# Performance work log

Hardware: AMD Instinct MI355X
Metric: run time of the kernel (lower is better)

The kernel has to match this reference:

```python
import jax, jax.numpy as jnp
import numpy as np
import math

B, S, E, H = 2, 8192, 1024, 16
D = E // H  # 64
CHUNK = 128


def _build_slopes(n):
    # ALiBi-style slopes (n is a power of 2 here)
    start = 2.0 ** (-(2.0 ** -(math.log2(n) - 3)))
    return np.array([start * (start ** i) for i in range(n)], dtype=np.float32)


def setup_inputs() -> dict:
    key = jax.random.key(0)
    ks = jax.random.split(key, 6)
    x = jax.random.normal(ks[0], (B, S, E), dtype=jnp.float32)
    # rotary table: (S, D//2, 2) = (cos, sin)
    inv_freq = 1.0 / (10000.0 ** (np.arange(0, D, 2, dtype=np.float32) / D))
    ang = np.arange(S, dtype=np.float32)[:, None] * inv_freq[None, :]  # (S, D/2)
    freqs_cis = jnp.asarray(np.stack([np.cos(ang), np.sin(ang)], axis=-1))
    wq = jax.random.normal(ks[1], (E, E), dtype=jnp.float32) * 0.02
    wk = jax.random.normal(ks[2], (E, E), dtype=jnp.float32) * 0.02
    wv = jax.random.normal(ks[3], (E, E), dtype=jnp.float32) * 0.02
    wo = jax.random.normal(ks[4], (E, E), dtype=jnp.float32) * 0.02
    rms_w = jnp.ones((E,), dtype=jnp.float32)
    return {"x": x, "freqs_cis": freqs_cis, "wq": wq, "wk": wk, "wv": wv, "wo": wo, "rms_w": rms_w}


def apply_rotary(x, fc):
    # x: (b, s, h, d); fc: (s, d/2, 2)
    xr = x.reshape(*x.shape[:-1], -1, 2)          # (b,s,h,d/2,2)
    fc = fc[None, :, None, :, :]                   # (1,s,1,d/2,2)
    out = jnp.stack([
        xr[..., 0] * fc[..., 0] - xr[..., 1] * fc[..., 1],
        xr[..., 1] * fc[..., 0] + xr[..., 0] * fc[..., 1],
    ], axis=-1)
    return out.reshape(x.shape)


def lightning_attn(q, k, v, slopes, C=CHUNK):
    # q,k,v: (B,H,S,D); per-head decay lambda = exp(-slope)
    Bs, Hs, Ss, Ds = q.shape
    NC = Ss // C
    j = jnp.arange(C, dtype=jnp.float32)
    diff = j[:, None] - j[None, :]
    s3 = slopes[:, None, None]                     # (H,1,1)
    Dmask = jnp.where(diff >= 0, jnp.exp(-s3 * diff), 0.0)   # (H,C,C) intra decay
    q_dec = jnp.exp(-slopes[:, None] * (j + 1.0))             # (H,C) cross-chunk q decay
    k_dec = jnp.exp(-slopes[:, None] * (C - 1.0 - j))         # (H,C) state-update k decay
    c_dec = jnp.exp(-slopes * C)[None, :, None, None]         # (1,H,1,1) full-chunk decay
    qc = q.reshape(Bs, Hs, NC, C, Ds).transpose(2, 0, 1, 3, 4)
    kc = k.reshape(Bs, Hs, NC, C, Ds).transpose(2, 0, 1, 3, 4)
    vc = v.reshape(Bs, Hs, NC, C, Ds).transpose(2, 0, 1, 3, 4)

    def step(St, inp):
        qb, kb, vb = inp                                       # (B,H,C,D)
        scores = jnp.einsum('bhid,bhjd->bhij', qb, kb) * Dmask[None]
        o = jnp.einsum('bhij,bhjd->bhid', scores, vb)
        o = o + q_dec[None, :, :, None] * jnp.einsum('bhid,bhde->bhie', qb, St)
        St = c_dec * St + jnp.einsum('bhcd,bhce->bhde', kb * k_dec[None, :, :, None], vb)
        return St, o

    S0 = jnp.zeros((Bs, Hs, Ds, Ds), dtype=jnp.float32)
    _, oc = jax.lax.scan(step, S0, (qc, kc, vc))               # oc: (NC,B,H,C,D)
    return oc.transpose(1, 2, 0, 3, 4).reshape(Bs, Hs, Ss, Ds)


def rms_norm(x, w, eps=1e-5):
    xf = x.astype(jnp.float32)
    n = xf * jax.lax.rsqrt(jnp.mean(xf * xf, axis=-1, keepdims=True) + eps)
    return n.astype(x.dtype) * w


def reference(x, freqs_cis, wq, wk, wv, wo, rms_w):
    b, s, _ = x.shape
    slopes = jnp.asarray(_build_slopes(H))
    q = (x @ wq.T).reshape(b, s, H, D)
    k = (x @ wk.T).reshape(b, s, H, D)
    v = (x @ wv.T).reshape(b, s, H, D)
    q = apply_rotary(q, freqs_cis)
    k = apply_rotary(k, freqs_cis)
    q = q.transpose(0, 2, 1, 3)   # (B,H,S,D)
    k = k.transpose(0, 2, 1, 3)
    v = v.transpose(0, 2, 1, 3)
    o = lightning_attn(q, k, v, slopes)             # (B,H,S,D)
    o = o.transpose(0, 2, 1, 3).reshape(b, s, E)    # b n (h d)
    o = rms_norm(o, rms_w)
    return o @ wo.T
```

## Files before the change

kernel.cpp:

```cpp
#include <hip/hip_runtime.h>


using h16   = _Float16;
using h16x8 = __attribute__((ext_vector_type(8))) _Float16;
using h16x4 = __attribute__((ext_vector_type(4))) _Float16;
using f32x4 = __attribute__((ext_vector_type(4))) float;

#define MFMA16(a,b,c) __builtin_amdgcn_mfma_f32_16x16x32_f16(a,b,c,0,0,0)

__device__ __forceinline__ h16x8 rope8(h16x8 v, const float* __restrict__ fp) {
  float4 f0 = *(const float4*)fp;
  float4 f1 = *(const float4*)(fp + 4);
  h16x8 o; float x0, x1;
  x0=(float)v[0]; x1=(float)v[1]; o[0]=(h16)(x0*f0.x - x1*f0.y); o[1]=(h16)(x1*f0.x + x0*f0.y);
  x0=(float)v[2]; x1=(float)v[3]; o[2]=(h16)(x0*f0.z - x1*f0.w); o[3]=(h16)(x1*f0.z + x0*f0.w);
  x0=(float)v[4]; x1=(float)v[5]; o[4]=(h16)(x0*f1.x - x1*f1.y); o[5]=(h16)(x1*f1.x + x0*f1.y);
  x0=(float)v[6]; x1=(float)v[7]; o[6]=(h16)(x0*f1.z - x1*f1.w); o[7]=(h16)(x1*f1.z + x0*f1.w);
  return o;
}

__global__ __launch_bounds__(256) void k_cvt(const float* __restrict__ s,
                                             h16* __restrict__ d, int n) {
  int i = (blockIdx.x * 256 + threadIdx.x) * 8;
  if (i >= n) return;
  float4 a = *(const float4*)(s + i);
  float4 b = *(const float4*)(s + i + 4);
  h16x8 o;
  o[0]=(h16)a.x; o[1]=(h16)a.y; o[2]=(h16)a.z; o[3]=(h16)a.w;
  o[4]=(h16)b.x; o[5]=(h16)b.y; o[6]=(h16)b.z; o[7]=(h16)b.w;
  *(h16x8*)(d + i) = o;
}

__global__ __launch_bounds__(256) void k_qkv(
    const h16* __restrict__ xh, const h16* __restrict__ w3,
    h16* __restrict__ qn, h16* __restrict__ kn, h16* __restrict__ vn)
{
  __shared__ __align__(16) h16 lA[128*64];
  __shared__ __align__(16) h16 lB[128*64];
  const int tid = threadIdx.x;
  const int m0 = blockIdx.x * 128;
  const int nt = blockIdx.y;
  const int n0 = nt * 128;
  const int w = tid >> 6, l = tid & 63;
  const int wr = w >> 1, wc = w & 1;
  const int sr = tid >> 3, sc = tid & 7;
  const int ssl = sc ^ (sr & 7);
  const h16* At = xh + (size_t)m0 * 1024;
  const h16* Bt = w3 + (size_t)n0 * 1024;

  f32x4 acc[4][4] = {};
  h16x8 ra[4], rb[4];
  #pragma unroll
  for (int i = 0; i < 4; i++) {
    ra[i] = *(const h16x8*)(At + (size_t)(i*32+sr)*1024 + sc*8);
    rb[i] = *(const h16x8*)(Bt + (size_t)(i*32+sr)*1024 + sc*8);
  }
  #pragma unroll
  for (int i = 0; i < 4; i++) {
    *(h16x8*)(lA + (i*32+sr)*64 + ssl*8) = ra[i];
    *(h16x8*)(lB + (i*32+sr)*64 + ssl*8) = rb[i];
  }
  __syncthreads();

  for (int kt = 0; kt < 16; ++kt) {
    if (kt < 15) {
      #pragma unroll
      for (int i = 0; i < 4; i++) {
        ra[i] = *(const h16x8*)(At + (size_t)(i*32+sr)*1024 + (kt+1)*64 + sc*8);
        rb[i] = *(const h16x8*)(Bt + (size_t)(i*32+sr)*1024 + (kt+1)*64 + sc*8);
      }
    }
    #pragma unroll
    for (int ks = 0; ks < 2; ++ks) {
      h16x8 af[4], bf[4];
      #pragma unroll
      for (int mf = 0; mf < 4; mf++) {
        int row = wr*64 + mf*16 + (l & 15);
        int slot = (ks*4 + (l >> 4)) ^ (row & 7);
        af[mf] = *(const h16x8*)(lA + row*64 + slot*8);
      }
      #pragma unroll
      for (int nf = 0; nf < 4; nf++) {
        int row = wc*64 + nf*16 + (l & 15);
        int slot = (ks*4 + (l >> 4)) ^ (row & 7);
        bf[nf] = *(const h16x8*)(lB + row*64 + slot*8);
      }
      #pragma unroll
      for (int mf = 0; mf < 4; mf++)
        #pragma unroll
        for (int nf = 0; nf < 4; nf++)
          acc[mf][nf] = MFMA16(af[mf], bf[nf], acc[mf][nf]);
    }
    __syncthreads();
    if (kt < 15) {
      #pragma unroll
      for (int i = 0; i < 4; i++) {
        *(h16x8*)(lA + (i*32+sr)*64 + ssl*8) = ra[i];
        *(h16x8*)(lB + (i*32+sr)*64 + ssl*8) = rb[i];
      }
    }
    __syncthreads();
  }

  const int proj = nt >> 3;
  h16* dst = proj == 0 ? qn : (proj == 1 ? kn : vn);
  const int cb = (nt & 7) * 128;
  #pragma unroll
  for (int mf = 0; mf < 4; mf++)
    #pragma unroll
    for (int nf = 0; nf < 4; nf++)
      #pragma unroll
      for (int r = 0; r < 4; r++) {
        int row = wr*64 + mf*16 + ((l >> 4) << 2) + r;
        int col = cb + wc*64 + nf*16 + (l & 15);
        dst[(size_t)(m0 + row)*1024 + col] = (h16)acc[mf][nf][r];
      }
}

__global__ __launch_bounds__(256) void k_out(
    const h16* __restrict__ an, const h16* __restrict__ woh,
    float* __restrict__ out)
{
  __shared__ __align__(16) h16 lA[128*64];
  __shared__ __align__(16) h16 lB[128*64];
  const int tid = threadIdx.x;
  const int m0 = blockIdx.x * 128;
  const int n0 = blockIdx.y * 128;
  const int w = tid >> 6, l = tid & 63;
  const int wr = w >> 1, wc = w & 1;
  const int sr = tid >> 3, sc = tid & 7;
  const int ssl = sc ^ (sr & 7);
  const h16* At = an + (size_t)m0 * 1024;
  const h16* Bt = woh + (size_t)n0 * 1024;

  f32x4 acc[4][4] = {};
  h16x8 ra[4], rb[4];
  #pragma unroll
  for (int i = 0; i < 4; i++) {
    ra[i] = *(const h16x8*)(At + (size_t)(i*32+sr)*1024 + sc*8);
    rb[i] = *(const h16x8*)(Bt + (size_t)(i*32+sr)*1024 + sc*8);
  }
  #pragma unroll
  for (int i = 0; i < 4; i++) {
    *(h16x8*)(lA + (i*32+sr)*64 + ssl*8) = ra[i];
    *(h16x8*)(lB + (i*32+sr)*64 + ssl*8) = rb[i];
  }
  __syncthreads();

  for (int kt = 0; kt < 16; ++kt) {
    if (kt < 15) {
      #pragma unroll
      for (int i = 0; i < 4; i++) {
        ra[i] = *(const h16x8*)(At + (size_t)(i*32+sr)*1024 + (kt+1)*64 + sc*8);
        rb[i] = *(const h16x8*)(Bt + (size_t)(i*32+sr)*1024 + (kt+1)*64 + sc*8);
      }
    }
    #pragma unroll
    for (int ks = 0; ks < 2; ++ks) {
      h16x8 af[4], bf[4];
      #pragma unroll
      for (int mf = 0; mf < 4; mf++) {
        int row = wr*64 + mf*16 + (l & 15);
        int slot = (ks*4 + (l >> 4)) ^ (row & 7);
        af[mf] = *(const h16x8*)(lA + row*64 + slot*8);
      }
      #pragma unroll
      for (int nf = 0; nf < 4; nf++) {
        int row = wc*64 + nf*16 + (l & 15);
        int slot = (ks*4 + (l >> 4)) ^ (row & 7);
        bf[nf] = *(const h16x8*)(lB + row*64 + slot*8);
      }
      #pragma unroll
      for (int mf = 0; mf < 4; mf++)
        #pragma unroll
        for (int nf = 0; nf < 4; nf++)
          acc[mf][nf] = MFMA16(af[mf], bf[nf], acc[mf][nf]);
    }
    __syncthreads();
    if (kt < 15) {
      #pragma unroll
      for (int i = 0; i < 4; i++) {
        *(h16x8*)(lA + (i*32+sr)*64 + ssl*8) = ra[i];
        *(h16x8*)(lB + (i*32+sr)*64 + ssl*8) = rb[i];
      }
    }
    __syncthreads();
  }
  #pragma unroll
  for (int mf = 0; mf < 4; mf++)
    #pragma unroll
    for (int nf = 0; nf < 4; nf++)
      #pragma unroll
      for (int r = 0; r < 4; r++) {
        int row = wr*64 + mf*16 + ((l >> 4) << 2) + r;
        int col = wc*64 + nf*16 + (l & 15);
        out[(size_t)(m0 + row)*1024 + n0 + col] = acc[mf][nf][r];
      }
}

__global__ __launch_bounds__(256) void k_tr(
    const h16* __restrict__ kn, const h16* __restrict__ vn,
    const float* __restrict__ fc,
    h16* __restrict__ kts, h16* __restrict__ vt)
{
  __shared__ __align__(16) h16 tl[128*64];
  __shared__ float dt[128];
  const int tid = threadIdx.x;
  const int st = blockIdx.x;
  const int bh = blockIdx.y;
  const int b = bh >> 4, h = bh & 15;
  if (tid < 128) {
    float slope = exp2f(-0.5f * (float)(h + 1));
    dt[tid] = expf(-slope * (float)(127 - tid));
  }
  const size_t ibase = ((size_t)(b*8192 + st*128))*1024 + h*64;
  const size_t obase = (size_t)bh*64*8192 + st*128;
  const int cr = tid >> 3, c8 = tid & 7;

  for (int which = 0; which < 2; ++which) {
    const h16* src = which ? vn : kn;
    h16* dstp = which ? vt : kts;
    __syncthreads();
    #pragma unroll
    for (int i = 0; i < 4; i++) {
      int r = i*32 + cr;
      h16x8 v = *(const h16x8*)(src + ibase + (size_t)r*1024 + c8*8);
      if (!which) v = rope8(v, fc + (size_t)(st*128 + r)*64 + c8*8);
      int slot = (c8 + ((r >> 3) & 7)) & 7;
      *(h16x8*)(tl + r*64 + slot*8) = v;
    }
    __syncthreads();
    #pragma unroll
    for (int i = 0; i < 4; i++) {
      int chunk = i*256 + tid;
      int d = chunk >> 4;
      int j8 = chunk & 15;
      h16x8 o;
      #pragma unroll
      for (int jj = 0; jj < 8; jj++) {
        int c = j8*8 + jj;
        int pos = (d + ((c >> 3) & 7)*8) & 63;
        float fv = (float)tl[c*64 + pos];
        if (!which) fv *= dt[c];
        o[jj] = (h16)fv;
      }
      *(h16x8*)(dstp + obase + (size_t)d*8192 + j8*8) = o;
    }
  }
}

__global__ __launch_bounds__(256) void k_kv(
    const h16* __restrict__ kts, const h16* __restrict__ vt,
    float* __restrict__ T)
{
  const int tid = threadIdx.x;
  const int t = blockIdx.x;
  const int bh = blockIdx.y;
  const int w = tid >> 6, l = tid & 63;
  const h16* vb = vt  + (size_t)bh*64*8192 + t*128;
  const h16* kb = kts + (size_t)bh*64*8192 + t*128;
  f32x4 acc[4] = {};
  h16x8 a[4];
  #pragma unroll
  for (int ks = 0; ks < 4; ks++)
    a[ks] = *(const h16x8*)(vb + (size_t)(w*16 + (l & 15))*8192 + ks*32 + (l >> 4)*8);
  #pragma unroll
  for (int nf = 0; nf < 4; nf++) {
    #pragma unroll
    for (int ks = 0; ks < 4; ks++) {
      h16x8 bfr = *(const h16x8*)(kb + (size_t)(nf*16 + (l & 15))*8192 + ks*32 + (l >> 4)*8);
      acc[nf] = MFMA16(a[ks], bfr, acc[nf]);
    }
  }
  float* Tb = T + ((size_t)bh*64 + t)*4096;
  #pragma unroll
  for (int nf = 0; nf < 4; nf++)
    #pragma unroll
    for (int r = 0; r < 4; r++) {
      int e = w*16 + ((l >> 4) << 2) + r;
      int d = nf*16 + (l & 15);
      Tb[e*64 + d] = acc[nf][r];
    }
}

__global__ __launch_bounds__(256) void k_scan(const float* __restrict__ T,
                                              h16* __restrict__ ph) {
  const int bh = blockIdx.x;
  const int j  = blockIdx.y * 256 + threadIdx.x;
  const int h = bh & 15;
  const float cdec = expf(-exp2f(-0.5f*(float)(h+1)) * 128.0f);
  const float* Tb = T + (size_t)bh*64*4096 + j;
  h16* pb = ph + (size_t)bh*64*4096 + j;
  float run = 0.f;
  for (int t = 0; t < 64; t++) {
    float kv = Tb[(size_t)t*4096];
    pb[(size_t)t*4096] = (h16)run;
    run = cdec*run + kv;
  }
}

__global__ __launch_bounds__(256) void k_att(
    const h16* __restrict__ qn, const h16* __restrict__ kn,
    const float* __restrict__ fc,
    const h16* __restrict__ vt, const h16* __restrict__ ph,
    h16* __restrict__ oh)
{
  __shared__ __align__(16) h16 P[128*144];
  __shared__ float dt[128], qd[128];
  const int tid = threadIdx.x;
  const int t = blockIdx.x;
  const int bh = blockIdx.y;
  const int b = bh >> 4, h = bh & 15;
  if (tid < 128) {
    float slope = exp2f(-0.5f*(float)(h+1));
    dt[tid] = expf(-slope*(float)tid);
    qd[tid] = expf(-slope*(float)(tid+1));
  }
  __syncthreads();
  const int w = tid >> 6, l = tid & 63;
  const int iw = w * 32;
  const h16* qb = qn + ((size_t)(b*8192 + t*128))*1024 + h*64;
  const h16* kb = kn + ((size_t)(b*8192 + t*128))*1024 + h*64;
  const h16* vb = vt + (size_t)bh*64*8192 + t*128;
  const h16* pb = ph + ((size_t)bh*64 + t)*4096;
  const float* fcb = fc + (size_t)(t*128)*64;

  h16x8 aq[2][2];
  #pragma unroll
  for (int mf = 0; mf < 2; mf++)
    #pragma unroll
    for (int ks = 0; ks < 2; ks++) {
      int row = iw + mf*16 + (l & 15);
      int d0 = ks*32 + (l >> 4)*8;
      aq[mf][ks] = rope8(*(const h16x8*)(qb + (size_t)row*1024 + d0),
                         fcb + (size_t)row*64 + d0);
    }

  f32x4 sc[2][8] = {};
  #pragma unroll
  for (int nf = 0; nf < 8; nf++) {
    if (nf*16 <= iw + 31) {
      #pragma unroll
      for (int ks = 0; ks < 2; ks++) {
        int row = nf*16 + (l & 15);
        int d0 = ks*32 + (l >> 4)*8;
        h16x8 bk = rope8(*(const h16x8*)(kb + (size_t)row*1024 + d0),
                         fcb + (size_t)row*64 + d0);
        sc[0][nf] = MFMA16(aq[0][ks], bk, sc[0][nf]);
        sc[1][nf] = MFMA16(aq[1][ks], bk, sc[1][nf]);
      }
    }
  }
  #pragma unroll
  for (int mf = 0; mf < 2; mf++) {
    #pragma unroll
    for (int nf = 0; nf < 8; nf++) {
      #pragma unroll
      for (int r = 0; r < 4; r++) {
        int i = iw + mf*16 + ((l >> 4) << 2) + r;
        int j = nf*16 + (l & 15);
        int diff = i - j;
        float v = diff >= 0 ? sc[mf][nf][r]*dt[diff] : 0.f;
        P[i*144 + j] = (h16)v;
      }
    }
  }
  f32x4 ao[2][4] = {};
  #pragma unroll
  for (int kc = 0; kc < 4; kc++) {
    h16x8 ap0 = *(const h16x8*)(P + (size_t)(iw + (l & 15))*144 + kc*32 + (l >> 4)*8);
    h16x8 ap1 = *(const h16x8*)(P + (size_t)(iw + 16 + (l & 15))*144 + kc*32 + (l >> 4)*8);
    #pragma unroll
    for (int nf = 0; nf < 4; nf++) {
      h16x8 bv = *(const h16x8*)(vb + (size_t)(nf*16 + (l & 15))*8192 + kc*32 + (l >> 4)*8);
      ao[0][nf] = MFMA16(ap0, bv, ao[0][nf]);
      ao[1][nf] = MFMA16(ap1, bv, ao[1][nf]);
    }
  }
  f32x4 a2[2][4] = {};
  #pragma unroll
  for (int ks = 0; ks < 2; ks++) {
    #pragma unroll
    for (int nf = 0; nf < 4; nf++) {
      h16x8 bs = *(const h16x8*)(pb + (size_t)(nf*16 + (l & 15))*64 + ks*32 + (l >> 4)*8);
      a2[0][nf] = MFMA16(aq[0][ks], bs, a2[0][nf]);
      a2[1][nf] = MFMA16(aq[1][ks], bs, a2[1][nf]);
    }
  }
  #pragma unroll
  for (int mf = 0; mf < 2; mf++) {
    #pragma unroll
    for (int nf = 0; nf < 4; nf++) {
      #pragma unroll
      for (int r = 0; r < 4; r++) {
        int i = iw + mf*16 + ((l >> 4) << 2) + r;
        int e = nf*16 + (l & 15);
        float o = ao[mf][nf][r] + qd[i]*a2[mf][nf][r];
        int s = t*128 + i;
        oh[((size_t)(b*8192 + s))*1024 + h*64 + e] = (h16)o;
      }
    }
  }
}

__global__ __launch_bounds__(256) void k_rms(const h16* __restrict__ o,
                                             const float* __restrict__ rw,
                                             h16* __restrict__ an) {
  const int tid = threadIdx.x;
  const size_t base = (size_t)blockIdx.x * 1024;
  h16x4 hv = *(const h16x4*)(o + base + tid*4);
  float v0 = (float)hv[0], v1 = (float)hv[1], v2 = (float)hv[2], v3 = (float)hv[3];
  float ss = v0*v0 + v1*v1 + v2*v2 + v3*v3;
  #pragma unroll
  for (int off = 32; off > 0; off >>= 1) ss += __shfl_down(ss, off);
  __shared__ float red[4];
  if ((tid & 63) == 0) red[tid >> 6] = ss;
  __syncthreads();
  float f = rsqrtf((red[0]+red[1]+red[2]+red[3]) * (1.0f/1024.0f) + 1e-5f);
  float4 wv = *(const float4*)(rw + tid*4);
  h16x4 r;
  r[0] = (h16)(v0*f*wv.x); r[1] = (h16)(v1*f*wv.y);
  r[2] = (h16)(v2*f*wv.z); r[3] = (h16)(v3*f*wv.w);
  *(h16x4*)(an + base + tid*4) = r;
}

extern "C" void kernel_launch(void* const* d_in, const int* in_sizes, int n_in,
                              void* d_out, int out_size, void* d_ws, size_t ws_size,
                              hipStream_t stream) {
  const float* x  = (const float*)d_in[0];
  const float* fc = (const float*)d_in[1];
  const float* wq = (const float*)d_in[2];
  const float* wk = (const float*)d_in[3];
  const float* wv = (const float*)d_in[4];
  const float* wo = (const float*)d_in[5];
  const float* rw = (const float*)d_in[6];
  float* out = (float*)d_out;

  char* p = (char*)d_ws;
  const size_t SZ = 33554432;
  h16* xh  = (h16*)(p);
  h16* vn  = (h16*)(p + 3*SZ);
  h16* kts = (h16*)(p + 4*SZ);
  h16* vt  = (h16*)(p + 5*SZ);
  float* T = (float*)(p + 6*SZ);
  h16* w3  = (h16*)(p + 7*SZ);
  h16* woh = (h16*)(p + 7*SZ + 6291456);
  h16* qn = (h16*)out;
  h16* kn = (h16*)out + 16777216;

  hipLaunchKernelGGL(k_cvt, dim3(8192), dim3(256), 0, stream, x, xh, 16777216);
  hipLaunchKernelGGL(k_cvt, dim3(512), dim3(256), 0, stream, wq, w3, 1048576);
  hipLaunchKernelGGL(k_cvt, dim3(512), dim3(256), 0, stream, wk, w3 + 1048576, 1048576);
  hipLaunchKernelGGL(k_cvt, dim3(512), dim3(256), 0, stream, wv, w3 + 2097152, 1048576);
  hipLaunchKernelGGL(k_cvt, dim3(512), dim3(256), 0, stream, wo, woh, 1048576);

  hipLaunchKernelGGL(k_qkv, dim3(128, 24), dim3(256), 0, stream, xh, w3, qn, kn, vn);
  hipLaunchKernelGGL(k_tr,  dim3(64, 32), dim3(256), 0, stream, kn, vn, fc, kts, vt);
  hipLaunchKernelGGL(k_kv,  dim3(64, 32), dim3(256), 0, stream, kts, vt, T);
  h16* ph = vn;
  hipLaunchKernelGGL(k_scan, dim3(32, 16), dim3(256), 0, stream, T, ph);
  h16* oh = (h16*)T;
  hipLaunchKernelGGL(k_att, dim3(64, 32), dim3(256), 0, stream, qn, kn, fc, vt, ph, oh);
  h16* an = xh;
  hipLaunchKernelGGL(k_rms, dim3(16384), dim3(256), 0, stream, oh, rw, an);
  hipLaunchKernelGGL(k_out, dim3(128, 8), dim3(256), 0, stream, an, woh, out);
}
```

Measured before the change: 348.4 us.

## Rewrite projection GEMMs with 256x256 tiles and async global-to-LDS double buffering

Replaces the 128x128, 256-thread QKV and output GEMMs with a shared 256x256-tile, 512-thread main loop. Operands go straight from global memory into LDS through global_load_lds, the 64-wide K tiles are double-buffered in 128KB of dynamic LDS, and the MFMA block runs at raised wave priority. The aim is more data reuse per tile and better overlap of memory loads with matrix math. The cost is one block per CU because of the LDS footprint, and only one wave of blocks for the output projection (64x4 grid).

```diff
diff --git a/kernel.cpp b/kernel.cpp
--- a/kernel.cpp
+++ b/kernel.cpp
@@ -7,6 +7,10 @@
 using f32x4 = __attribute__((ext_vector_type(4))) float;
 
 #define MFMA16(a,b,c) __builtin_amdgcn_mfma_f32_16x16x32_f16(a,b,c,0,0,0)
+
+#define GLOAD16(gp, lp) __builtin_amdgcn_global_load_lds( \
+    (const __attribute__((address_space(1))) void*)(gp),  \
+    (__attribute__((address_space(3))) void*)(lp), 16, 0, 0)
 
 __device__ __forceinline__ h16x8 rope8(h16x8 v, const float* __restrict__ fp) {
   float4 f0 = *(const float4*)fp;
@@ -31,170 +35,132 @@
   *(h16x8*)(d + i) = o;
 }
 
-__global__ __launch_bounds__(256) void k_qkv(
+__device__ __forceinline__ void gemm256_loop(
+    const h16* __restrict__ At, const h16* __restrict__ Bt,
+    char* smem, int w, int l, f32x4 (&acc)[8][4])
+{
+  char* lA = smem;
+  char* lB = smem + 65536;
+  const int wr = w >> 2, wc = w & 3;
+  const int rl = l >> 3;
+  const int sl8 = ((l & 7) ^ rl) * 8;
+
+  auto stage = [&](int kt) {
+    const int kb = (kt & 1) * 32768;
+    #pragma unroll
+    for (int half = 0; half < 2; half++) {
+      #pragma unroll
+      for (int c = 0; c < 2; c++) {
+        const int r = half*128 + (c*8 + w)*8 + rl;
+        const int dof = kb + half*16384 + (c*8 + w)*1024;
+        GLOAD16(At + (size_t)r*1024 + kt*64 + sl8, lA + dof);
+        GLOAD16(Bt + (size_t)r*1024 + kt*64 + sl8, lB + dof);
+      }
+    }
+  };
+
+  const int foff0 = (((l >> 4)    ) ^ (l & 7)) * 16;
+  const int foff1 = (((l >> 4) + 4) ^ (l & 7)) * 16;
+  const int abyte = wr*16384 + (l & 15)*128;
+  const int bbyte = (wc >> 1)*16384 + ((wc & 1)*64 + (l & 15))*128;
+
+  stage(0); stage(1);
+  asm volatile("s_waitcnt vmcnt(8)" ::: "memory");
+  __builtin_amdgcn_sched_barrier(0);
+  __builtin_amdgcn_s_barrier();
+
+  for (int t = 0; t < 16; ++t) {
+    const int kb = (t & 1) * 32768;
+    const char* aB = lA + kb + abyte;
+    const char* bB = lB + kb + bbyte;
+    h16x8 af0[8], af1[8], bf0[4], bf1[4];
+    #pragma unroll
+    for (int mf = 0; mf < 8; mf++) {
+      af0[mf] = *(const h16x8*)(aB + mf*2048 + foff0);
+      af1[mf] = *(const h16x8*)(aB + mf*2048 + foff1);
+    }
+    #pragma unroll
+    for (int nf = 0; nf < 4; nf++) {
+      bf0[nf] = *(const h16x8*)(bB + nf*2048 + foff0);
+      bf1[nf] = *(const h16x8*)(bB + nf*2048 + foff1);
+    }
+    asm volatile("s_waitcnt lgkmcnt(0)" ::: "memory");
+    __builtin_amdgcn_sched_barrier(0);
+    __builtin_amdgcn_s_barrier();
+    if (t < 14) stage(t + 2);
+    __builtin_amdgcn_s_setprio(1);
+    #pragma unroll
+    for (int mf = 0; mf < 8; mf++)
+      #pragma unroll
+      for (int nf = 0; nf < 4; nf++)
+        acc[mf][nf] = MFMA16(af0[mf], bf0[nf], acc[mf][nf]);
+    #pragma unroll
+    for (int mf = 0; mf < 8; mf++)
+      #pragma unroll
+      for (int nf = 0; nf < 4; nf++)
+        acc[mf][nf] = MFMA16(af1[mf], bf1[nf], acc[mf][nf]);
+    __builtin_amdgcn_s_setprio(0);
+    if (t < 14)       asm volatile("s_waitcnt vmcnt(8)" ::: "memory");
+    else if (t == 14) asm volatile("s_waitcnt vmcnt(0)" ::: "memory");
+    if (t < 15) {
+      __builtin_amdgcn_sched_barrier(0);
+      __builtin_amdgcn_s_barrier();
+    }
+  }
+}
+
+__global__ __launch_bounds__(512, 2) void k_qkv(
     const h16* __restrict__ xh, const h16* __restrict__ w3,
     h16* __restrict__ qn, h16* __restrict__ kn, h16* __restrict__ vn)
 {
-  __shared__ __align__(16) h16 lA[128*64];
-  __shared__ __align__(16) h16 lB[128*64];
-  const int tid = threadIdx.x;
-  const int m0 = blockIdx.x * 128;
+  extern __shared__ __align__(16) char smem[];
+  const int tid = threadIdx.x;
+  const int w = tid >> 6, l = tid & 63;
+  const int m0 = blockIdx.x * 256;
   const int nt = blockIdx.y;
-  const int n0 = nt * 128;
-  const int w = tid >> 6, l = tid & 63;
-  const int wr = w >> 1, wc = w & 1;
-  const int sr = tid >> 3, sc = tid & 7;
-  const int ssl = sc ^ (sr & 7);
-  const h16* At = xh + (size_t)m0 * 1024;
-  const h16* Bt = w3 + (size_t)n0 * 1024;
-
-  f32x4 acc[4][4] = {};
-  h16x8 ra[4], rb[4];
-  #pragma unroll
-  for (int i = 0; i < 4; i++) {
-    ra[i] = *(const h16x8*)(At + (size_t)(i*32+sr)*1024 + sc*8);
-    rb[i] = *(const h16x8*)(Bt + (size_t)(i*32+sr)*1024 + sc*8);
-  }
-  #pragma unroll
-  for (int i = 0; i < 4; i++) {
-    *(h16x8*)(lA + (i*32+sr)*64 + ssl*8) = ra[i];
-    *(h16x8*)(lB + (i*32+sr)*64 + ssl*8) = rb[i];
-  }
-  __syncthreads();
-
-  for (int kt = 0; kt < 16; ++kt) {
-    if (kt < 15) {
-      #pragma unroll
-      for (int i = 0; i < 4; i++) {
-        ra[i] = *(const h16x8*)(At + (size_t)(i*32+sr)*1024 + (kt+1)*64 + sc*8);
-        rb[i] = *(const h16x8*)(Bt + (size_t)(i*32+sr)*1024 + (kt+1)*64 + sc*8);
-      }
-    }
-    #pragma unroll
-    for (int ks = 0; ks < 2; ++ks) {
-      h16x8 af[4], bf[4];
-      #pragma unroll
-      for (int mf = 0; mf < 4; mf++) {
-        int row = wr*64 + mf*16 + (l & 15);
-        int slot = (ks*4 + (l >> 4)) ^ (row & 7);
-        af[mf] = *(const h16x8*)(lA + row*64 + slot*8);
-      }
-      #pragma unroll
-      for (int nf = 0; nf < 4; nf++) {
-        int row = wc*64 + nf*16 + (l & 15);
-        int slot = (ks*4 + (l >> 4)) ^ (row & 7);
-        bf[nf] = *(const h16x8*)(lB + row*64 + slot*8);
-      }
-      #pragma unroll
-      for (int mf = 0; mf < 4; mf++)
-        #pragma unroll
-        for (int nf = 0; nf < 4; nf++)
-          acc[mf][nf] = MFMA16(af[mf], bf[nf], acc[mf][nf]);
-    }
-    __syncthreads();
-    if (kt < 15) {
-      #pragma unroll
-      for (int i = 0; i < 4; i++) {
-        *(h16x8*)(lA + (i*32+sr)*64 + ssl*8) = ra[i];
-        *(h16x8*)(lB + (i*32+sr)*64 + ssl*8) = rb[i];
-      }
-    }
-    __syncthreads();
-  }
-
-  const int proj = nt >> 3;
+  const int wr = w >> 2, wc = w & 3;
+
+  f32x4 acc[8][4] = {};
+  gemm256_loop(xh + (size_t)m0*1024, w3 + (size_t)(nt*256)*1024, smem, w, l, acc);
+
+  const int proj = nt >> 2;
   h16* dst = proj == 0 ? qn : (proj == 1 ? kn : vn);
-  const int cb = (nt & 7) * 128;
-  #pragma unroll
-  for (int mf = 0; mf < 4; mf++)
+  const int cb = (nt & 3)*256 + wc*64;
+  #pragma unroll
+  for (int mf = 0; mf < 8; mf++)
     #pragma unroll
     for (int nf = 0; nf < 4; nf++)
       #pragma unroll
       for (int r = 0; r < 4; r++) {
-        int row = wr*64 + mf*16 + ((l >> 4) << 2) + r;
-        int col = cb + wc*64 + nf*16 + (l & 15);
+        int row = wr*128 + mf*16 + ((l >> 4) << 2) + r;
+        int col = cb + nf*16 + (l & 15);
         dst[(size_t)(m0 + row)*1024 + col] = (h16)acc[mf][nf][r];
       }
 }
 
-__global__ __launch_bounds__(256) void k_out(
+__global__ __launch_bounds__(512, 2) void k_out(
     const h16* __restrict__ an, const h16* __restrict__ woh,
     float* __restrict__ out)
 {
-  __shared__ __align__(16) h16 lA[128*64];
-  __shared__ __align__(16) h16 lB[128*64];
-  const int tid = threadIdx.x;
-  const int m0 = blockIdx.x * 128;
-  const int n0 = blockIdx.y * 128;
+  extern __shared__ __align__(16) char smem[];
+  const int tid = threadIdx.x;
   const int w = tid >> 6, l = tid & 63;
-  const int wr = w >> 1, wc = w & 1;
-  const int sr = tid >> 3, sc = tid & 7;
-  const int ssl = sc ^ (sr & 7);
-  const h16* At = an + (size_t)m0 * 1024;
-  const h16* Bt = woh + (size_t)n0 * 1024;
-
-  f32x4 acc[4][4] = {};
-  h16x8 ra[4], rb[4];
-  #pragma unroll
-  for (int i = 0; i < 4; i++) {
-    ra[i] = *(const h16x8*)(At + (size_t)(i*32+sr)*1024 + sc*8);
-    rb[i] = *(const h16x8*)(Bt + (size_t)(i*32+sr)*1024 + sc*8);
-  }
-  #pragma unroll
-  for (int i = 0; i < 4; i++) {
-    *(h16x8*)(lA + (i*32+sr)*64 + ssl*8) = ra[i];
-    *(h16x8*)(lB + (i*32+sr)*64 + ssl*8) = rb[i];
-  }
-  __syncthreads();
-
-  for (int kt = 0; kt < 16; ++kt) {
-    if (kt < 15) {
-      #pragma unroll
-      for (int i = 0; i < 4; i++) {
-        ra[i] = *(const h16x8*)(At + (size_t)(i*32+sr)*1024 + (kt+1)*64 + sc*8);
-        rb[i] = *(const h16x8*)(Bt + (size_t)(i*32+sr)*1024 + (kt+1)*64 + sc*8);
-      }
-    }
-    #pragma unroll
-    for (int ks = 0; ks < 2; ++ks) {
-      h16x8 af[4], bf[4];
-      #pragma unroll
-      for (int mf = 0; mf < 4; mf++) {
-        int row = wr*64 + mf*16 + (l & 15);
-        int slot = (ks*4 + (l >> 4)) ^ (row & 7);
-        af[mf] = *(const h16x8*)(lA + row*64 + slot*8);
-      }
-      #pragma unroll
-      for (int nf = 0; nf < 4; nf++) {
-        int row = wc*64 + nf*16 + (l & 15);
-        int slot = (ks*4 + (l >> 4)) ^ (row & 7);
-        bf[nf] = *(const h16x8*)(lB + row*64 + slot*8);
-      }
-      #pragma unroll
-      for (int mf = 0; mf < 4; mf++)
-        #pragma unroll
-        for (int nf = 0; nf < 4; nf++)
-          acc[mf][nf] = MFMA16(af[mf], bf[nf], acc[mf][nf]);
-    }
-    __syncthreads();
-    if (kt < 15) {
-      #pragma unroll
-      for (int i = 0; i < 4; i++) {
-        *(h16x8*)(lA + (i*32+sr)*64 + ssl*8) = ra[i];
-        *(h16x8*)(lB + (i*32+sr)*64 + ssl*8) = rb[i];
-      }
-    }
-    __syncthreads();
-  }
-  #pragma unroll
-  for (int mf = 0; mf < 4; mf++)
+  const int m0 = blockIdx.x * 256;
+  const int n0 = blockIdx.y * 256;
+  const int wr = w >> 2, wc = w & 3;
+
+  f32x4 acc[8][4] = {};
+  gemm256_loop(an + (size_t)m0*1024, woh + (size_t)n0*1024, smem, w, l, acc);
+
+  #pragma unroll
+  for (int mf = 0; mf < 8; mf++)
     #pragma unroll
     for (int nf = 0; nf < 4; nf++)
       #pragma unroll
       for (int r = 0; r < 4; r++) {
-        int row = wr*64 + mf*16 + ((l >> 4) << 2) + r;
-        int col = wc*64 + nf*16 + (l & 15);
-        out[(size_t)(m0 + row)*1024 + n0 + col] = acc[mf][nf][r];
+        int row = wr*128 + mf*16 + ((l >> 4) << 2) + r;
+        int col = n0 + wc*64 + nf*16 + (l & 15);
+        out[(size_t)(m0 + row)*1024 + col] = acc[mf][nf][r];
       }
 }
 
@@ -448,13 +414,16 @@
   h16* qn = (h16*)out;
   h16* kn = (h16*)out + 16777216;
 
+  (void)hipFuncSetAttribute((const void*)k_qkv, hipFuncAttributeMaxDynamicSharedMemorySize, 131072);
+  (void)hipFuncSetAttribute((const void*)k_out, hipFuncAttributeMaxDynamicSharedMemorySize, 131072);
+
   hipLaunchKernelGGL(k_cvt, dim3(8192), dim3(256), 0, stream, x, xh, 16777216);
   hipLaunchKernelGGL(k_cvt, dim3(512), dim3(256), 0, stream, wq, w3, 1048576);
   hipLaunchKernelGGL(k_cvt, dim3(512), dim3(256), 0, stream, wk, w3 + 1048576, 1048576);
   hipLaunchKernelGGL(k_cvt, dim3(512), dim3(256), 0, stream, wv, w3 + 2097152, 1048576);
   hipLaunchKernelGGL(k_cvt, dim3(512), dim3(256), 0, stream, wo, woh, 1048576);
 
-  hipLaunchKernelGGL(k_qkv, dim3(128, 24), dim3(256), 0, stream, xh, w3, qn, kn, vn);
+  hipLaunchKernelGGL(k_qkv, dim3(64, 12), dim3(512), 131072, stream, xh, w3, qn, kn, vn);
   hipLaunchKernelGGL(k_tr,  dim3(64, 32), dim3(256), 0, stream, kn, vn, fc, kts, vt);
   hipLaunchKernelGGL(k_kv,  dim3(64, 32), dim3(256), 0, stream, kts, vt, T);
   h16* ph = vn;
@@ -463,5 +432,5 @@
   hipLaunchKernelGGL(k_att, dim3(64, 32), dim3(256), 0, stream, qn, kn, fc, vt, ph, oh);
   h16* an = xh;
   hipLaunchKernelGGL(k_rms, dim3(16384), dim3(256), 0, stream, oh, rw, an);
-  hipLaunchKernelGGL(k_out, dim3(128, 8), dim3(256), 0, stream, an, woh, out);
-}
+  hipLaunchKernelGGL(k_out, dim3(64, 4), dim3(512), 131072, stream, an, woh, out);
+}
```

Result: faster. 318.2 us (-8.7%).
